# Kernel tuning notes

Measured on AMD Instinct MI355X. Metric: run time of the kernel, lower is better.

Reference implementation:

```python
import jax, jax.numpy as jnp
import numpy as np

B, L, H, D = 2, 2048, 16, 64


def setup_inputs() -> dict:
    key = jax.random.key(0)
    k1, k2, k3, k4 = jax.random.split(key, 4)
    query_states = jax.random.normal(k1, (B, L, H, D), dtype=jnp.float32)
    key_states = jax.random.normal(k2, (B, L, H, D), dtype=jnp.float32)
    # per-head linear feature maps (LinearFeatureMap parameters)
    Wq = jax.random.normal(k3, (H, D, D), dtype=jnp.float32)
    Wk = jax.random.normal(k4, (H, D, D), dtype=jnp.float32)
    return {"query_states": query_states, "key_states": key_states, "Wq": Wq, "Wk": Wk}


def reference(query_states, key_states, Wq, Wk):
    # per-head linear feature map: [B,L,H,D] x [H,D,E] -> [B,L,H,E]
    q = jnp.einsum('blhd,hde->blhe', query_states, Wq)
    k = jnp.einsum('blhd,hde->blhe', key_states, Wk)
    # kernelized attention scores: [B,H,L,S]
    attn = jnp.einsum('blhd,bshd->bhls', q, k)
    # sum-normalization over keys (non-softmax normalizer)
    attn = attn / jnp.sum(attn, axis=-1, keepdims=True)
    return attn
```

## Files before the change

### kernel.cpp

```cpp
#include <hip/hip_runtime.h>
#include <stdint.h>

#define NB 2
#define NL 2048
#define NH 16
#define ND 64

typedef __attribute__((ext_vector_type(8))) short short8;
typedef __attribute__((ext_vector_type(4))) float f32x4;
typedef __attribute__((ext_vector_type(4))) unsigned short ushort4v;

__device__ __forceinline__ unsigned short f2bf_rne(float x) {
    union { float f; unsigned int u; } v; v.f = x;
    unsigned int r = v.u + 0x7fffu + ((v.u >> 16) & 1u);
    return (unsigned short)(r >> 16);
}
__device__ __forceinline__ float bf2f(unsigned short b) {
    union { unsigned int u; float f; } v; v.u = ((unsigned int)b) << 16;
    return v.f;
}

__global__ __launch_bounds__(256) void pre_kernel(const float* __restrict__ query,
                                                  const float* __restrict__ key,
                                                  const float* __restrict__ Wq,
                                                  const float* __restrict__ Wk,
                                                  unsigned short* __restrict__ qbh,
                                                  unsigned short* __restrict__ qbl,
                                                  unsigned short* __restrict__ kbh,
                                                  unsigned short* __restrict__ kbl,
                                                  double* __restrict__ part) {
    __shared__ __align__(16) char lds_raw[16384 + 34816];
    const int blk = blockIdx.x;
    const int t = threadIdx.x;

    if (blk < 1024) {
        const bool isq = blk < 512;
        const int pb = isq ? blk : blk - 512;
        const float* x = isq ? query : key;
        const float* W = isq ? Wq : Wk;
        unsigned short* ph = isq ? qbh : kbh;
        unsigned short* pl = isq ? qbl : kbl;
        float* Wlds = (float*)lds_raw;
        float* xs = (float*)(lds_raw + 16384);

        const int lc = pb & 15;
        const int h = (pb >> 4) & 15;
        const int b = pb >> 8;
        const int l0 = lc * 128;

        {
            const float4* src = (const float4*)(W + (size_t)h * ND * ND);
#pragma unroll
            for (int i = 0; i < 4; ++i)
                ((float4*)Wlds)[t + 256 * i] = src[t + 256 * i];
        }
        {
#pragma unroll
            for (int i = 0; i < 8; ++i) {
                const int idx = t + 256 * i;
                const int r = idx >> 4, c = idx & 15;
                const float4 v = *(const float4*)(x + (((size_t)b * NL + l0 + r) * NH + h) * ND + c * 4);
                *(float4*)&xs[r * 68 + c * 4] = v;
            }
        }
        __syncthreads();

        const int e4 = (t & 15) * 4;
        const int rg = t >> 4;
        float acc[8][4] = {};
        for (int d = 0; d < ND; ++d) {
            const float4 w4 = *(const float4*)&Wlds[d * ND + e4];
#pragma unroll
            for (int it = 0; it < 8; ++it) {
                const float xv = xs[(rg + it * 16) * 68 + d];
                acc[it][0] += xv * w4.x; acc[it][1] += xv * w4.y;
                acc[it][2] += xv * w4.z; acc[it][3] += xv * w4.w;
            }
        }

        unsigned short* phh = ph + ((size_t)(b * NH + h) * NL + l0) * ND;
        unsigned short* pll = pl + ((size_t)(b * NH + h) * NL + l0) * ND;
#pragma unroll
        for (int it = 0; it < 8; ++it) {
            const int r = rg + it * 16;
            const int ep = e4 ^ ((r & 7) << 3);
            ushort4v hv, lv;
#pragma unroll
            for (int j = 0; j < 4; ++j) {
                const unsigned short hb = f2bf_rne(acc[it][j]);
                hv[j] = hb;
                lv[j] = f2bf_rne(acc[it][j] - bf2f(hb));
            }
            *(ushort4v*)&phh[(size_t)r * ND + ep] = hv;
            *(ushort4v*)&pll[(size_t)r * ND + ep] = lv;
        }
    } else {
        double (*red)[64] = (double(*)[64])lds_raw;
        const int blk2 = blk - 1024;
        const int chunk = blk2 & 15, bh = blk2 >> 4;
        const int b = bh >> 4, h = bh & 15;
        const int e = t & 63, sub = t >> 6;
        const float* base = key + ((size_t)b * NL * NH + h) * ND + e;
        double acc = 0.0;
        const int s0 = chunk * 128 + sub * 32;
        for (int s = s0; s < s0 + 32; ++s)
            acc += (double)base[(size_t)s * (NH * ND)];
        red[sub][e] = acc;
        __syncthreads();
        if (t < 64) {
            const double s2 = red[0][t] + red[1][t] + red[2][t] + red[3][t];
            part[(size_t)blk2 * 64 + t] = s2;
        }
    }
}

__global__ __launch_bounds__(64) void prep_kernel(const double* __restrict__ part,
                                                  const float* __restrict__ Wq,
                                                  const float* __restrict__ Wk,
                                                  double* __restrict__ v) {
    __shared__ double xs[ND], ks[ND];
    const int bh = blockIdx.x;
    const int h = bh & 15;
    const int t = threadIdx.x;
    {
        double a = 0.0;
#pragma unroll
        for (int c = 0; c < 16; ++c) a += part[((size_t)bh * 16 + c) * 64 + t];
        xs[t] = a;
    }
    __syncthreads();
    {
        double acc = 0.0;
        const float* wk = Wk + (size_t)h * ND * ND + t;
        for (int d = 0; d < ND; ++d) acc += xs[d] * (double)wk[(size_t)d * ND];
        ks[t] = acc;
    }
    __syncthreads();
    {
        double acc = 0.0;
        const float* wq = Wq + (size_t)h * ND * ND + (size_t)t * ND;
        for (int e = 0; e < ND; ++e) acc += (double)wq[e] * ks[e];
        v[(size_t)bh * ND + t] = acc;
    }
}

__global__ __launch_bounds__(256) void den_kernel(const float* __restrict__ xq,
                                                  const double* __restrict__ v,
                                                  float* __restrict__ invden) {
    __shared__ double vs[ND];
    const int bh = blockIdx.x;
    const int b = bh >> 4, h = bh & 15;
    const int t = threadIdx.x;
    if (t < 64) vs[t] = v[(size_t)bh * ND + t];
    __syncthreads();
    const int l = blockIdx.y * 256 + t;
    const float* xp = xq + (((size_t)b * NL + l) * NH + h) * ND;
    double acc = 0.0;
#pragma unroll 8
    for (int d = 0; d < ND; ++d) acc += (double)xp[d] * vs[d];
    invden[(size_t)bh * NL + l] = (float)(1.0 / acc);
}

__global__ __launch_bounds__(256, 4) void attn_kernel(const unsigned short* __restrict__ qbh,
                                                      const unsigned short* __restrict__ qbl,
                                                      const unsigned short* __restrict__ kbh,
                                                      const unsigned short* __restrict__ kbl,
                                                      const float* __restrict__ invden,
                                                      float* __restrict__ out) {
    __shared__ unsigned short smem[2 * 128 * 64];
    const int lg = blockIdx.x;
    const int s0 = blockIdx.y * 128;
    const int bh = blockIdx.z;
    const int t = threadIdx.x;
    const int w = t >> 6, ln = t & 63;

    {
        const size_t pan = (size_t)bh * NL * ND;
        const unsigned short* srcs[2] = {kbh + pan + (size_t)s0 * ND,
                                         kbl + pan + (size_t)s0 * ND};
#pragma unroll
        for (int arr = 0; arr < 2; ++arr) {
            const unsigned short* s = srcs[arr] + w * 2048 + ln * 8;
            unsigned short* d = smem + arr * 8192 + w * 2048;
#pragma unroll
            for (int u = 0; u < 4; ++u) {
                __builtin_amdgcn_global_load_lds((const __attribute__((address_space(1))) unsigned int*)(s + u * 512),
                                                 (__attribute__((address_space(3))) unsigned int*)(d + u * 512),
                                                 16, 0, 0);
            }
        }
    }
    __syncthreads();

    const int wr = w >> 1, wc = w & 1;
    const int fr = ln & 15, g = ln >> 4;
    const int swz = (fr & 7) << 4;
    const int cofs0 = (g << 4) ^ swz;
    const int cofs1 = (64 | (g << 4)) ^ swz;
    const char* sb = (const char*)smem;
    const char* qh_pb = (const char*)(qbh + (size_t)bh * NL * ND);
    const char* ql_pb = (const char*)(qbl + (size_t)bh * NL * ND);

    for (int tile = 0; tile < 4; ++tile) {
        const int l0 = lg * 512 + tile * 128;
        const int lbase = l0 + wc * 64 + fr;

        short8 qh_f[4][2], ql_f[4][2];
#pragma unroll
        for (int j = 0; j < 4; ++j) {
            const size_t roff = (size_t)(lbase + j * 16) * 128;
            qh_f[j][0] = *(const short8*)(qh_pb + roff + cofs0);
            qh_f[j][1] = *(const short8*)(qh_pb + roff + cofs1);
            ql_f[j][0] = *(const short8*)(ql_pb + roff + cofs0);
            ql_f[j][1] = *(const short8*)(ql_pb + roff + cofs1);
        }
        const float* invp = invden + (size_t)bh * NL + lbase;
        float invs[4];
#pragma unroll
        for (int j = 0; j < 4; ++j) invs[j] = invp[j * 16];

#pragma unroll
        for (int i = 0; i < 4; ++i) {
            const int arow = wr * 64 + i * 16 + fr;
            const short8 kh0 = *(const short8*)(sb + arow * 128 + cofs0);
            const short8 kh1 = *(const short8*)(sb + arow * 128 + cofs1);
            const short8 kl0 = *(const short8*)(sb + 16384 + arow * 128 + cofs0);
            const short8 kl1 = *(const short8*)(sb + 16384 + arow * 128 + cofs1);
#pragma unroll
            for (int j = 0; j < 4; ++j) {
                f32x4 a = (f32x4){0.f, 0.f, 0.f, 0.f};
                a = __builtin_amdgcn_mfma_f32_16x16x32_bf16(kh0, qh_f[j][0], a, 0, 0, 0);
                a = __builtin_amdgcn_mfma_f32_16x16x32_bf16(kh0, ql_f[j][0], a, 0, 0, 0);
                a = __builtin_amdgcn_mfma_f32_16x16x32_bf16(kl0, qh_f[j][0], a, 0, 0, 0);
                a = __builtin_amdgcn_mfma_f32_16x16x32_bf16(kh1, qh_f[j][1], a, 0, 0, 0);
                a = __builtin_amdgcn_mfma_f32_16x16x32_bf16(kh1, ql_f[j][1], a, 0, 0, 0);
                a = __builtin_amdgcn_mfma_f32_16x16x32_bf16(kl1, qh_f[j][1], a, 0, 0, 0);
                const float inv = invs[j];
                f32x4 vv = a;
                vv[0] *= inv; vv[1] *= inv; vv[2] *= inv; vv[3] *= inv;
                *(f32x4*)(out + ((size_t)bh * NL + lbase + j * 16) * NL + s0 + wr * 64 + g * 4 + i * 16) = vv;
            }
        }
    }
}

extern "C" void kernel_launch(void* const* d_in, const int* in_sizes, int n_in,
                              void* d_out, int out_size, void* d_ws, size_t ws_size,
                              hipStream_t stream) {
    const float* query = (const float*)d_in[0];
    const float* key   = (const float*)d_in[1];
    const float* Wq    = (const float*)d_in[2];
    const float* Wk    = (const float*)d_in[3];
    float* out = (float*)d_out;

    const size_t npan = (size_t)NB * NH * NL * ND;
    char* ws = (char*)d_ws;
    unsigned short* qbh = (unsigned short*)(ws);
    unsigned short* qbl = (unsigned short*)(ws + 1 * npan * 2);
    unsigned short* kbh = (unsigned short*)(ws + 2 * npan * 2);
    unsigned short* kbl = (unsigned short*)(ws + 3 * npan * 2);
    double* part  = (double*)(ws + 4 * npan * 2);
    double* v     = (double*)(ws + 4 * npan * 2 + 262144);
    float* invden = (float*)(ws + 4 * npan * 2 + 262144 + 16384);

    pre_kernel<<<1536, 256, 0, stream>>>(query, key, Wq, Wk, qbh, qbl, kbh, kbl, part);
    prep_kernel<<<NB * NH, 64, 0, stream>>>(part, Wq, Wk, v);
    den_kernel<<<dim3(NB * NH, NL / 256), 256, 0, stream>>>(query, v, invden);
    attn_kernel<<<dim3(4, 16, NB * NH), 256, 0, stream>>>(qbh, qbl, kbh, kbl, invden, out);
}
```

Before: 189.5 us.

## Fuse prep into den kernel and double-buffer Q fragments in attention loop

The small per-head prep kernel is folded into the denominator kernel, so each block recomputes the projected key-sum vector itself and one launch plus a global round-trip are removed. In the attention kernel, the Q hi/lo fragments and inverse denominators are loaded in half-tiles of 32 rows into a two-slot register buffer. The next half-tile is prefetched while MFMAs run on the current one, to hide global load latency. The costs are redundant double-precision prep work across the 8 blocks per head and register pressure from the double buffer.

```diff
diff --git a/kernel.cpp b/kernel.cpp
--- a/kernel.cpp
+++ b/kernel.cpp
@@ -114,44 +114,35 @@
     }
 }
 
-__global__ __launch_bounds__(64) void prep_kernel(const double* __restrict__ part,
+__global__ __launch_bounds__(256) void den_kernel(const float* __restrict__ xq,
+                                                  const double* __restrict__ part,
                                                   const float* __restrict__ Wq,
                                                   const float* __restrict__ Wk,
-                                                  double* __restrict__ v) {
-    __shared__ double xs[ND], ks[ND];
+                                                  float* __restrict__ invden) {
+    __shared__ double xs[ND], ks[ND], vs[ND];
     const int bh = blockIdx.x;
-    const int h = bh & 15;
+    const int b = bh >> 4, h = bh & 15;
     const int t = threadIdx.x;
-    {
+    if (t < 64) {
         double a = 0.0;
 #pragma unroll
         for (int c = 0; c < 16; ++c) a += part[((size_t)bh * 16 + c) * 64 + t];
         xs[t] = a;
     }
     __syncthreads();
-    {
+    if (t < 64) {
         double acc = 0.0;
         const float* wk = Wk + (size_t)h * ND * ND + t;
         for (int d = 0; d < ND; ++d) acc += xs[d] * (double)wk[(size_t)d * ND];
         ks[t] = acc;
     }
     __syncthreads();
-    {
+    if (t < 64) {
         double acc = 0.0;
         const float* wq = Wq + (size_t)h * ND * ND + (size_t)t * ND;
         for (int e = 0; e < ND; ++e) acc += (double)wq[e] * ks[e];
-        v[(size_t)bh * ND + t] = acc;
-    }
-}
-
-__global__ __launch_bounds__(256) void den_kernel(const float* __restrict__ xq,
-                                                  const double* __restrict__ v,
-                                                  float* __restrict__ invden) {
-    __shared__ double vs[ND];
-    const int bh = blockIdx.x;
-    const int b = bh >> 4, h = bh & 15;
-    const int t = threadIdx.x;
-    if (t < 64) vs[t] = v[(size_t)bh * ND + t];
+        vs[t] = acc;
+    }
     __syncthreads();
     const int l = blockIdx.y * 256 + t;
     const float* xp = xq + (((size_t)b * NL + l) * NH + h) * ND;
@@ -200,25 +191,41 @@
     const char* sb = (const char*)smem;
     const char* qh_pb = (const char*)(qbh + (size_t)bh * NL * ND);
     const char* ql_pb = (const char*)(qbl + (size_t)bh * NL * ND);
-
-    for (int tile = 0; tile < 4; ++tile) {
-        const int l0 = lg * 512 + tile * 128;
-        const int lbase = l0 + wc * 64 + fr;
-
-        short8 qh_f[4][2], ql_f[4][2];
-#pragma unroll
-        for (int j = 0; j < 4; ++j) {
-            const size_t roff = (size_t)(lbase + j * 16) * 128;
-            qh_f[j][0] = *(const short8*)(qh_pb + roff + cofs0);
-            qh_f[j][1] = *(const short8*)(qh_pb + roff + cofs1);
-            ql_f[j][0] = *(const short8*)(ql_pb + roff + cofs0);
-            ql_f[j][1] = *(const short8*)(ql_pb + roff + cofs1);
-        }
-        const float* invp = invden + (size_t)bh * NL + lbase;
-        float invs[4];
-#pragma unroll
-        for (int j = 0; j < 4; ++j) invs[j] = invp[j * 16];
-
+    const float* invb = invden + (size_t)bh * NL;
+
+    short8 qf[2][2][2][2];
+    float invv[2][2];
+
+    {
+        const int lb = lg * 512 + wc * 64 + fr;
+#pragma unroll
+        for (int j = 0; j < 2; ++j) {
+            const size_t roff = (size_t)(lb + j * 16) * 128;
+            qf[0][j][0][0] = *(const short8*)(qh_pb + roff + cofs0);
+            qf[0][j][0][1] = *(const short8*)(qh_pb + roff + cofs1);
+            qf[0][j][1][0] = *(const short8*)(ql_pb + roff + cofs0);
+            qf[0][j][1][1] = *(const short8*)(ql_pb + roff + cofs1);
+            invv[0][j] = invb[lb + j * 16];
+        }
+    }
+
+#pragma unroll
+    for (int ht = 0; ht < 8; ++ht) {
+        const int cur = ht & 1, nxt = cur ^ 1;
+        if (ht < 7) {
+            const int h2 = ht + 1;
+            const int lb = lg * 512 + (h2 >> 1) * 128 + wc * 64 + (h2 & 1) * 32 + fr;
+#pragma unroll
+            for (int j = 0; j < 2; ++j) {
+                const size_t roff = (size_t)(lb + j * 16) * 128;
+                qf[nxt][j][0][0] = *(const short8*)(qh_pb + roff + cofs0);
+                qf[nxt][j][0][1] = *(const short8*)(qh_pb + roff + cofs1);
+                qf[nxt][j][1][0] = *(const short8*)(ql_pb + roff + cofs0);
+                qf[nxt][j][1][1] = *(const short8*)(ql_pb + roff + cofs1);
+                invv[nxt][j] = invb[lb + j * 16];
+            }
+        }
+        const int lbc = lg * 512 + (ht >> 1) * 128 + wc * 64 + (ht & 1) * 32 + fr;
 #pragma unroll
         for (int i = 0; i < 4; ++i) {
             const int arow = wr * 64 + i * 16 + fr;
@@ -227,18 +234,18 @@
             const short8 kl0 = *(const short8*)(sb + 16384 + arow * 128 + cofs0);
             const short8 kl1 = *(const short8*)(sb + 16384 + arow * 128 + cofs1);
 #pragma unroll
-            for (int j = 0; j < 4; ++j) {
+            for (int j = 0; j < 2; ++j) {
                 f32x4 a = (f32x4){0.f, 0.f, 0.f, 0.f};
-                a = __builtin_amdgcn_mfma_f32_16x16x32_bf16(kh0, qh_f[j][0], a, 0, 0, 0);
-                a = __builtin_amdgcn_mfma_f32_16x16x32_bf16(kh0, ql_f[j][0], a, 0, 0, 0);
-                a = __builtin_amdgcn_mfma_f32_16x16x32_bf16(kl0, qh_f[j][0], a, 0, 0, 0);
-                a = __builtin_amdgcn_mfma_f32_16x16x32_bf16(kh1, qh_f[j][1], a, 0, 0, 0);
-                a = __builtin_amdgcn_mfma_f32_16x16x32_bf16(kh1, ql_f[j][1], a, 0, 0, 0);
-                a = __builtin_amdgcn_mfma_f32_16x16x32_bf16(kl1, qh_f[j][1], a, 0, 0, 0);
-                const float inv = invs[j];
+                a = __builtin_amdgcn_mfma_f32_16x16x32_bf16(kh0, qf[cur][j][0][0], a, 0, 0, 0);
+                a = __builtin_amdgcn_mfma_f32_16x16x32_bf16(kh0, qf[cur][j][1][0], a, 0, 0, 0);
+                a = __builtin_amdgcn_mfma_f32_16x16x32_bf16(kl0, qf[cur][j][0][0], a, 0, 0, 0);
+                a = __builtin_amdgcn_mfma_f32_16x16x32_bf16(kh1, qf[cur][j][0][1], a, 0, 0, 0);
+                a = __builtin_amdgcn_mfma_f32_16x16x32_bf16(kh1, qf[cur][j][1][1], a, 0, 0, 0);
+                a = __builtin_amdgcn_mfma_f32_16x16x32_bf16(kl1, qf[cur][j][0][1], a, 0, 0, 0);
+                const float inv = invv[cur][j];
                 f32x4 vv = a;
                 vv[0] *= inv; vv[1] *= inv; vv[2] *= inv; vv[3] *= inv;
-                *(f32x4*)(out + ((size_t)bh * NL + lbase + j * 16) * NL + s0 + wr * 64 + g * 4 + i * 16) = vv;
+                *(f32x4*)(out + ((size_t)bh * NL + lbc + j * 16) * NL + s0 + wr * 64 + g * 4 + i * 16) = vv;
             }
         }
     }
@@ -260,11 +267,9 @@
     unsigned short* kbh = (unsigned short*)(ws + 2 * npan * 2);
     unsigned short* kbl = (unsigned short*)(ws + 3 * npan * 2);
     double* part  = (double*)(ws + 4 * npan * 2);
-    double* v     = (double*)(ws + 4 * npan * 2 + 262144);
-    float* invden = (float*)(ws + 4 * npan * 2 + 262144 + 16384);
+    float* invden = (float*)(ws + 4 * npan * 2 + 262144);
 
     pre_kernel<<<1536, 256, 0, stream>>>(query, key, Wq, Wk, qbh, qbl, kbh, kbl, part);
-    prep_kernel<<<NB * NH, 64, 0, stream>>>(part, Wq, Wk, v);
-    den_kernel<<<dim3(NB * NH, NL / 256), 256, 0, stream>>>(query, v, invden);
+    den_kernel<<<dim3(NB * NH, NL / 256), 256, 0, stream>>>(query, part, Wq, Wk, invden);
     attn_kernel<<<dim3(4, 16, NB * NH), 256, 0, stream>>>(qbh, qbl, kbh, kbl, invden, out);
 }
```

Result: slower. 211.6 us (+11.7%).

## Stream K chunks through double-buffered LDS in persistent per-strip attention blocks

Applied to the files above, without the earlier changes.

The attention kernel is restructured so each 512-thread block owns a 256-row query strip of one head. It keeps its Q fragments and inverse denominators in registers and streams all keys in 64-row chunks through a double-buffered LDS stage, using async global-to-LDS loads and vmcnt waits. This replaces a grid of many small blocks that each reloaded Q and K tiles, with the aim of cutting redundant loads and overlapping K prefetch with MFMA and output stores. The cost is that the grid shrinks to 256 blocks at one block per CU, so fewer waves are available to hide the very large output write traffic.

```diff
diff --git a/kernel.cpp b/kernel.cpp
--- a/kernel.cpp
+++ b/kernel.cpp
@@ -161,87 +161,112 @@
     invden[(size_t)bh * NL + l] = (float)(1.0 / acc);
 }
 
-__global__ __launch_bounds__(256, 4) void attn_kernel(const unsigned short* __restrict__ qbh,
+__global__ __launch_bounds__(512, 1) void attn_kernel(const unsigned short* __restrict__ qbh,
                                                       const unsigned short* __restrict__ qbl,
                                                       const unsigned short* __restrict__ kbh,
                                                       const unsigned short* __restrict__ kbl,
                                                       const float* __restrict__ invden,
                                                       float* __restrict__ out) {
-    __shared__ unsigned short smem[2 * 128 * 64];
-    const int lg = blockIdx.x;
-    const int s0 = blockIdx.y * 128;
-    const int bh = blockIdx.z;
+    __shared__ unsigned short kbuf[2][2][64 * 64];
+    const int strip = blockIdx.x;
+    const int bh = blockIdx.y;
+    const int l0 = strip * 256;
     const int t = threadIdx.x;
     const int w = t >> 6, ln = t & 63;
-
-    {
-        const size_t pan = (size_t)bh * NL * ND;
-        const unsigned short* srcs[2] = {kbh + pan + (size_t)s0 * ND,
-                                         kbl + pan + (size_t)s0 * ND};
-#pragma unroll
-        for (int arr = 0; arr < 2; ++arr) {
-            const unsigned short* s = srcs[arr] + w * 2048 + ln * 8;
-            unsigned short* d = smem + arr * 8192 + w * 2048;
-#pragma unroll
-            for (int u = 0; u < 4; ++u) {
-                __builtin_amdgcn_global_load_lds((const __attribute__((address_space(1))) unsigned int*)(s + u * 512),
-                                                 (__attribute__((address_space(3))) unsigned int*)(d + u * 512),
-                                                 16, 0, 0);
-            }
-        }
-    }
-    __syncthreads();
-
-    const int wr = w >> 1, wc = w & 1;
     const int fr = ln & 15, g = ln >> 4;
     const int swz = (fr & 7) << 4;
     const int cofs0 = (g << 4) ^ swz;
     const int cofs1 = (64 | (g << 4)) ^ swz;
-    const char* sb = (const char*)smem;
-    const char* qh_pb = (const char*)(qbh + (size_t)bh * NL * ND);
-    const char* ql_pb = (const char*)(qbl + (size_t)bh * NL * ND);
-
-    for (int tile = 0; tile < 4; ++tile) {
-        const int l0 = lg * 512 + tile * 128;
-        const int lbase = l0 + wc * 64 + fr;
-
-        short8 qh_f[4][2], ql_f[4][2];
-#pragma unroll
-        for (int j = 0; j < 4; ++j) {
-            const size_t roff = (size_t)(lbase + j * 16) * 128;
-            qh_f[j][0] = *(const short8*)(qh_pb + roff + cofs0);
-            qh_f[j][1] = *(const short8*)(qh_pb + roff + cofs1);
-            ql_f[j][0] = *(const short8*)(ql_pb + roff + cofs0);
-            ql_f[j][1] = *(const short8*)(ql_pb + roff + cofs1);
-        }
-        const float* invp = invden + (size_t)bh * NL + lbase;
-        float invs[4];
-#pragma unroll
-        for (int j = 0; j < 4; ++j) invs[j] = invp[j * 16];
-
-#pragma unroll
-        for (int i = 0; i < 4; ++i) {
-            const int arow = wr * 64 + i * 16 + fr;
-            const short8 kh0 = *(const short8*)(sb + arow * 128 + cofs0);
-            const short8 kh1 = *(const short8*)(sb + arow * 128 + cofs1);
-            const short8 kl0 = *(const short8*)(sb + 16384 + arow * 128 + cofs0);
-            const short8 kl1 = *(const short8*)(sb + 16384 + arow * 128 + cofs1);
-#pragma unroll
-            for (int j = 0; j < 4; ++j) {
+
+    const size_t pan = (size_t)bh * NL * ND;
+    const unsigned short* kh_p = kbh + pan;
+    const unsigned short* kl_p = kbl + pan;
+    const char* qh_pb = (const char*)(qbh + pan);
+    const char* ql_pb = (const char*)(qbl + pan);
+    const int lbase = l0 + w * 32;
+
+    short8 qf00, qf01, qf10, qf11, qg00, qg01, qg10, qg11;
+    {
+        const size_t r0 = (size_t)(lbase + fr) * 128;
+        const size_t r1 = (size_t)(lbase + 16 + fr) * 128;
+        qf00 = *(const short8*)(qh_pb + r0 + cofs0);
+        qf01 = *(const short8*)(qh_pb + r0 + cofs1);
+        qf10 = *(const short8*)(ql_pb + r0 + cofs0);
+        qf11 = *(const short8*)(ql_pb + r0 + cofs1);
+        qg00 = *(const short8*)(qh_pb + r1 + cofs0);
+        qg01 = *(const short8*)(qh_pb + r1 + cofs1);
+        qg10 = *(const short8*)(ql_pb + r1 + cofs0);
+        qg11 = *(const short8*)(ql_pb + r1 + cofs1);
+    }
+    const float inv0 = invden[(size_t)bh * NL + lbase + fr];
+    const float inv1 = invden[(size_t)bh * NL + lbase + 16 + fr];
+
+#define STAGE(c, buf)                                                                              \
+    {                                                                                              \
+        const int u0 = w * 2;                                                                      \
+        _Pragma("unroll")                                                                          \
+        for (int qq = 0; qq < 2; ++qq) {                                                           \
+            const int u = u0 + qq;                                                                 \
+            const unsigned short* src = (u < 8) ? (kh_p + (size_t)(c) * 4096 + u * 512 + ln * 8)   \
+                                                : (kl_p + (size_t)(c) * 4096 + (u - 8) * 512 + ln * 8); \
+            unsigned short* dst = (u < 8) ? &kbuf[buf][0][u * 512] : &kbuf[buf][1][(u - 8) * 512]; \
+            __builtin_amdgcn_global_load_lds((const __attribute__((address_space(1))) unsigned int*)src, \
+                                             (__attribute__((address_space(3))) unsigned int*)dst, \
+                                             16, 0, 0);                                            \
+        }                                                                                          \
+    }
+
+    STAGE(0, 0);
+    asm volatile("s_waitcnt vmcnt(0)" ::: "memory");
+    __builtin_amdgcn_sched_barrier(0);
+    __builtin_amdgcn_s_barrier();
+
+    for (int c = 0; c < 32; ++c) {
+        const int cur = c & 1;
+        if (c < 31) STAGE(c + 1, cur ^ 1);
+
+        const char* kh_b = (const char*)kbuf[cur][0];
+        const char* kl_b = (const char*)kbuf[cur][1];
+#pragma unroll
+        for (int is = 0; is < 4; ++is) {
+            const int soff = (is * 16 + fr) * 128;
+            const short8 kh0 = *(const short8*)(kh_b + soff + cofs0);
+            const short8 kh1 = *(const short8*)(kh_b + soff + cofs1);
+            const short8 kl0 = *(const short8*)(kl_b + soff + cofs0);
+            const short8 kl1 = *(const short8*)(kl_b + soff + cofs1);
+            {
                 f32x4 a = (f32x4){0.f, 0.f, 0.f, 0.f};
-                a = __builtin_amdgcn_mfma_f32_16x16x32_bf16(kh0, qh_f[j][0], a, 0, 0, 0);
-                a = __builtin_amdgcn_mfma_f32_16x16x32_bf16(kh0, ql_f[j][0], a, 0, 0, 0);
-                a = __builtin_amdgcn_mfma_f32_16x16x32_bf16(kl0, qh_f[j][0], a, 0, 0, 0);
-                a = __builtin_amdgcn_mfma_f32_16x16x32_bf16(kh1, qh_f[j][1], a, 0, 0, 0);
-                a = __builtin_amdgcn_mfma_f32_16x16x32_bf16(kh1, ql_f[j][1], a, 0, 0, 0);
-                a = __builtin_amdgcn_mfma_f32_16x16x32_bf16(kl1, qh_f[j][1], a, 0, 0, 0);
-                const float inv = invs[j];
+                a = __builtin_amdgcn_mfma_f32_16x16x32_bf16(kh0, qf00, a, 0, 0, 0);
+                a = __builtin_amdgcn_mfma_f32_16x16x32_bf16(kh0, qf10, a, 0, 0, 0);
+                a = __builtin_amdgcn_mfma_f32_16x16x32_bf16(kl0, qf00, a, 0, 0, 0);
+                a = __builtin_amdgcn_mfma_f32_16x16x32_bf16(kh1, qf01, a, 0, 0, 0);
+                a = __builtin_amdgcn_mfma_f32_16x16x32_bf16(kh1, qf11, a, 0, 0, 0);
+                a = __builtin_amdgcn_mfma_f32_16x16x32_bf16(kl1, qf01, a, 0, 0, 0);
                 f32x4 vv = a;
-                vv[0] *= inv; vv[1] *= inv; vv[2] *= inv; vv[3] *= inv;
-                *(f32x4*)(out + ((size_t)bh * NL + lbase + j * 16) * NL + s0 + wr * 64 + g * 4 + i * 16) = vv;
-            }
-        }
-    }
+                vv[0] *= inv0; vv[1] *= inv0; vv[2] *= inv0; vv[3] *= inv0;
+                *(f32x4*)(out + ((size_t)bh * NL + lbase + fr) * NL + c * 64 + is * 16 + g * 4) = vv;
+            }
+            {
+                f32x4 a = (f32x4){0.f, 0.f, 0.f, 0.f};
+                a = __builtin_amdgcn_mfma_f32_16x16x32_bf16(kh0, qg00, a, 0, 0, 0);
+                a = __builtin_amdgcn_mfma_f32_16x16x32_bf16(kh0, qg10, a, 0, 0, 0);
+                a = __builtin_amdgcn_mfma_f32_16x16x32_bf16(kl0, qg00, a, 0, 0, 0);
+                a = __builtin_amdgcn_mfma_f32_16x16x32_bf16(kh1, qg01, a, 0, 0, 0);
+                a = __builtin_amdgcn_mfma_f32_16x16x32_bf16(kh1, qg11, a, 0, 0, 0);
+                a = __builtin_amdgcn_mfma_f32_16x16x32_bf16(kl1, qg01, a, 0, 0, 0);
+                f32x4 vv = a;
+                vv[0] *= inv1; vv[1] *= inv1; vv[2] *= inv1; vv[3] *= inv1;
+                *(f32x4*)(out + ((size_t)bh * NL + lbase + 16 + fr) * NL + c * 64 + is * 16 + g * 4) = vv;
+            }
+        }
+
+        if (c < 31) {
+            asm volatile("s_waitcnt vmcnt(8)" ::: "memory");
+            __builtin_amdgcn_sched_barrier(0);
+            __builtin_amdgcn_s_barrier();
+        }
+    }
+#undef STAGE
 }
 
 extern "C" void kernel_launch(void* const* d_in, const int* in_sizes, int n_in,
@@ -266,5 +291,5 @@
     pre_kernel<<<1536, 256, 0, stream>>>(query, key, Wq, Wk, qbh, qbl, kbh, kbl, part);
     prep_kernel<<<NB * NH, 64, 0, stream>>>(part, Wq, Wk, v);
     den_kernel<<<dim3(NB * NH, NL / 256), 256, 0, stream>>>(query, v, invden);
-    attn_kernel<<<dim3(4, 16, NB * NH), 256, 0, stream>>>(qbh, qbl, kbh, kbl, invden, out);
-}
+    attn_kernel<<<dim3(8, NB * NH), 512, 0, stream>>>(qbh, qbl, kbh, kbl, invden, out);
+}
```

Result: no change. 185.9 us (-1.9%).
